# Kernel optimization log

Measured on AMD Instinct MI355X. Metric: run time of the kernel, lower is better.

## Reference

```python
import jax, jax.numpy as jnp
import numpy as np

IGNORE_INDEX = -100
LABEL_SMOOTH = 0.1
GAMMA = 2.0
MARGIN = 0.6
SENTENCE_SCALE = 0.1
K = 1000000.0
VOCAB = 32000
B, T = 4, 512


def setup_inputs() -> dict:
    key = jax.random.key(0)
    k1, k2, k3, k4 = jax.random.split(key, 4)
    inp = jax.random.normal(k1, (B, VOCAB, T), dtype=jnp.float32)
    weight = jax.random.uniform(k2, (VOCAB,), dtype=jnp.float32)
    target = jax.random.randint(k3, (B, T), 0, VOCAB, dtype=jnp.int64)
    seq_len = jax.random.randint(k4, (B,), 1, T, dtype=jnp.int64)
    return {"input": inp, "weight": weight, "target": target, "seq_len": seq_len}


def reference(input, weight, target, seq_len):
    V = weight.shape[0]
    b, t = target.shape
    # log-softmax / softmax over vocab dim (axis=1) -- single stable pass
    logp = jax.nn.log_softmax(input, axis=1)          # (B, V, T)
    prob = jnp.exp(logp)                              # == softmax(input, dim=1)
    tgt = target[:, None, :]                          # (B, 1, T)
    # probability of the gold token at each position
    occur_prob = jnp.take_along_axis(prob, tgt, axis=1)[:, 0, :]   # (B, T)
    # predicted token and correctness
    pred = jnp.argmax(input, axis=1)                  # (B, T)
    pred_true = pred == target
    # token occurrence counts (scatter-add) and correct-prediction counts
    flat_tgt = target.reshape(-1)
    all_count = jnp.zeros((V,), jnp.int32).at[flat_tgt].add(1)
    true_count = jnp.zeros((V,), jnp.int32).at[flat_tgt].add(pred_true.reshape(-1).astype(jnp.int32))
    all_count = all_count.at[IGNORE_INDEX].set(0)     # negative index, matches torch
    true_count = true_count.at[IGNORE_INDEX].set(0)
    # label-smoothed cross entropy
    nll = -jnp.take_along_axis(logp, tgt, axis=1)[:, 0, :]          # (B, T)
    false_mean = (-jnp.sum(logp, axis=1) - nll) / (V - 1)           # mean over non-target classes
    ignore_mask = (target != IGNORE_INDEX).astype(logp.dtype)
    loss = (nll * (1.0 - LABEL_SMOOTH) + false_mean * LABEL_SMOOTH) * ignore_mask
    # per-token class weight (max_scale_rate > 0 branch)
    loss = loss * weight[target]
    # focal factor
    loss = loss * (1.0 - occur_prob) ** GAMMA
    # sentence weight (sentence_scale < 1 branch)
    pad = jnp.arange(t)[None, :] >= seq_len[:, None]                # (B, T) padding mask
    sw = jax.nn.sigmoid(K * (MARGIN - occur_prob))
    sw = jnp.where(pad, 0.0, sw).max(axis=1)
    sw = jnp.clip(sw, SENTENCE_SCALE, 1.0)
    loss = loss * sw[:, None]
    return loss, true_count, all_count
```

## Files before the change

### kernel.cpp

```cpp
#include <hip/hip_runtime.h>
#include <math.h>

#define IGNORE_INDEX (-100)
constexpr int Bn   = 4;
constexpr int T    = 512;
constexpr int V    = 32000;
constexpr int COLS = Bn * T;
constexpr int NCH  = 256;
constexpr int CHUNK = V / NCH;
constexpr float LS     = 0.1f;
constexpr float MARGIN = 0.6f;
constexpr float SSCALE = 0.1f;
constexpr float KBIG   = 1000000.0f;

typedef float floatx2 __attribute__((ext_vector_type(2)));

__global__ __launch_bounds__(256) void kA(const float* __restrict__ in,
                                          float4* __restrict__ part,
                                          float* __restrict__ cnt_base) {
    int tg = blockIdx.x * 256 + threadIdx.x;
    if (tg < 2 * V) cnt_base[tg] = 0.f;

    int j  = tg >> 10;
    int g  = tg & 1023;
    int b  = g >> 8;
    int t  = (g & 255) << 1;

    const float* base = in + ((size_t)b * V + (size_t)j * CHUNK) * T + t;

    float m0 = -INFINITY, m1 = -INFINITY;
    float s0 = 0.f, s1 = 0.f;
    float x0 = 0.f, x1 = 0.f;
    int   i0 = 0, i1 = 0;

    int vbase = j * CHUNK;
    for (int i = 0; i < CHUNK - 5; i += 10) {
        floatx2 vv[10];
#pragma unroll
        for (int u = 0; u < 10; ++u)
            vv[u] = __builtin_nontemporal_load((const floatx2*)(base + (size_t)(i + u) * T));
#pragma unroll
        for (int u = 0; u < 10; ++u) {
            floatx2 v = vv[u];
            int vi = vbase + i + u;
            s0 += __expf(v.x); if (v.x > m0) { m0 = v.x; i0 = vi; } x0 += v.x;
            s1 += __expf(v.y); if (v.y > m1) { m1 = v.y; i1 = vi; } x1 += v.y;
        }
    }
    {
        floatx2 vv[5];
#pragma unroll
        for (int u = 0; u < 5; ++u)
            vv[u] = __builtin_nontemporal_load((const floatx2*)(base + (size_t)(120 + u) * T));
#pragma unroll
        for (int u = 0; u < 5; ++u) {
            floatx2 v = vv[u];
            int vi = vbase + 120 + u;
            s0 += __expf(v.x); if (v.x > m0) { m0 = v.x; i0 = vi; } x0 += v.x;
            s1 += __expf(v.y); if (v.y > m1) { m1 = v.y; i1 = vi; } x1 += v.y;
        }
    }

    int c0 = g * 2;
    part[(size_t)(c0 + 0) * NCH + j] = make_float4(m0, s0, x0, __int_as_float(i0));
    part[(size_t)(c0 + 1) * NCH + j] = make_float4(m1, s1, x1, __int_as_float(i1));
}

__device__ __forceinline__ float4 merge(float4 a, float4 b) {
    float m = fmaxf(a.x, b.x);
    int idx = (b.x > a.x) ? __float_as_int(b.w) : __float_as_int(a.w);
    return make_float4(m, a.y + b.y, a.z + b.z, __int_as_float(idx));
}

__global__ __launch_bounds__(64) void kB(const float4* __restrict__ part,
                                         const float* __restrict__ in,
                                         const float* __restrict__ wgt,
                                         const int*   __restrict__ tgt,
                                         float* __restrict__ loss_base,
                                         float* __restrict__ sig_arr,
                                         float* __restrict__ cnt_true,
                                         float* __restrict__ cnt_all) {
    int c   = blockIdx.x;
    int tid = threadIdx.x;

    int tg  = tgt[c];
    int b   = c >> 9;
    int t   = c & 511;
    int tgc = (tg < 0) ? 0 : tg;
    float xt = in[((size_t)b * V + (size_t)tgc) * T + t];
    float w  = wgt[tgc];

    const float4* p = part + (size_t)c * NCH + tid * 4;
    float4 r = merge(merge(p[0], p[1]), merge(p[2], p[3]));

#pragma unroll
    for (int off = 32; off > 0; off >>= 1) {
        float mx = __shfl_down(r.x, off, 64);
        float sy = __shfl_down(r.y, off, 64);
        float sz = __shfl_down(r.z, off, 64);
        float iw = __shfl_down(r.w, off, 64);
        float m  = fmaxf(r.x, mx);
        int  idx = (mx > r.x) ? __float_as_int(iw) : __float_as_int(r.w);
        r = make_float4(m, r.y + sy, r.z + sz, __int_as_float(idx));
    }

    if (tid == 0) {
        float s = r.y, sumx = r.z;
        int pred = __float_as_int(r.w);

        float Z = __logf(s);
        float xv = (tg == IGNORE_INDEX) ? 0.f : xt;
        float nll = Z - xv;
        float occur = __expf(xv - Z);
        float sum_logp = sumx - (float)V * Z;
        float false_mean = (-sum_logp - nll) / (float)(V - 1);

        float mask = (tg != IGNORE_INDEX) ? 1.f : 0.f;
        float ww = (tg == IGNORE_INDEX) ? 0.f : w;
        float om = 1.f - occur;
        float loss = (nll * (1.f - LS) + false_mean * LS) * mask * ww * om * om;
        loss_base[c] = loss;

        if (tg != IGNORE_INDEX) {
            atomicAdd(&cnt_all[tg], 1.0f);
            if (pred == tg) atomicAdd(&cnt_true[tg], 1.0f);
        }

        float z = KBIG * (MARGIN - occur);
        float sig = (z >= 0.f) ? 1.f / (1.f + __expf(-z))
                               : __expf(z) / (1.f + __expf(z));
        sig_arr[c] = sig;
    }
}

__global__ __launch_bounds__(512) void kC(const float* __restrict__ loss_base,
                                          const float* __restrict__ sig_arr,
                                          const int*   __restrict__ slen,
                                          float* __restrict__ out) {
    __shared__ float red[8];
    int b = blockIdx.x;
    int t = threadIdx.x;
    int c = (b << 9) + t;

    float v = (t < slen[b]) ? sig_arr[c] : 0.f;
#pragma unroll
    for (int off = 32; off > 0; off >>= 1)
        v = fmaxf(v, __shfl_down(v, off, 64));
    if ((t & 63) == 0) red[t >> 6] = v;
    __syncthreads();
    if (t == 0) {
        float m = red[0];
#pragma unroll
        for (int i = 1; i < 8; ++i) m = fmaxf(m, red[i]);
        red[0] = fminf(fmaxf(m, SSCALE), 1.0f);
    }
    __syncthreads();
    float sw = red[0];
    out[c] = loss_base[c] * sw;

    if (b == 0 && t == 0) {
        out[COLS + (V + IGNORE_INDEX)] = 0.f;
        out[COLS + V + (V + IGNORE_INDEX)] = 0.f;
    }
}

extern "C" void kernel_launch(void* const* d_in, const int* in_sizes, int n_in,
                              void* d_out, int out_size, void* d_ws, size_t ws_size,
                              hipStream_t stream) {
    const float* inp  = (const float*)d_in[0];
    const float* wgt  = (const float*)d_in[1];
    const int*   tgt  = (const int*)d_in[2];
    const int*   slen = (const int*)d_in[3];

    float* out = (float*)d_out;
    float* cnt_true = out + COLS;
    float* cnt_all  = out + COLS + V;

    float4* part = (float4*)d_ws;
    float* loss_base = (float*)((char*)d_ws + (size_t)COLS * NCH * sizeof(float4));
    float* sig_arr   = loss_base + COLS;

    kA<<<(COLS / 2) * NCH / 256, 256, 0, stream>>>(inp, part, cnt_true);
    kB<<<COLS, 64, 0, stream>>>(part, inp, wgt, tgt,
                                loss_base, sig_arr, cnt_true, cnt_all);
    kC<<<Bn, 512, 0, stream>>>(loss_base, sig_arr, slen, out);
}
```

Before: 343.4 us.

## Widen loads to float4 per thread, use 64-row chunks with double-buffered loads

Each kA thread now handles four adjacent columns with 16-byte nontemporal loads over 64-row vocab chunks, software-pipelined across two 8-deep register buffers. Vocab is split into 500 real chunks padded to 512, with neutral partials written for the padding. kB merges 8 partials per lane instead of 4. This aims to raise memory-load efficiency and overlap loads with exp/argmax math. In exchange it doubles the partials buffer, adds more partial traffic, and raises register pressure.

```diff
diff --git a/kernel.cpp b/kernel.cpp
--- a/kernel.cpp
+++ b/kernel.cpp
@@ -6,64 +6,86 @@
 constexpr int T    = 512;
 constexpr int V    = 32000;
 constexpr int COLS = Bn * T;
-constexpr int NCH  = 256;
-constexpr int CHUNK = V / NCH;
+constexpr int NCHR = 500;
+constexpr int NCHP = 512;
+constexpr int CH   = 64;
 constexpr float LS     = 0.1f;
 constexpr float MARGIN = 0.6f;
 constexpr float SSCALE = 0.1f;
 constexpr float KBIG   = 1000000.0f;
 
-typedef float floatx2 __attribute__((ext_vector_type(2)));
-
-__global__ __launch_bounds__(256) void kA(const float* __restrict__ in,
-                                          float4* __restrict__ part,
-                                          float* __restrict__ cnt_base) {
+typedef float floatx4 __attribute__((ext_vector_type(4)));
+
+__global__ __launch_bounds__(256, 4) void kA(const float* __restrict__ in,
+                                             floatx4* __restrict__ part,
+                                             float* __restrict__ cnt_base) {
     int tg = blockIdx.x * 256 + threadIdx.x;
     if (tg < 2 * V) cnt_base[tg] = 0.f;
 
-    int j  = tg >> 10;
-    int g  = tg & 1023;
-    int b  = g >> 8;
-    int t  = (g & 255) << 1;
-
-    const float* base = in + ((size_t)b * V + (size_t)j * CHUNK) * T + t;
-
-    float m0 = -INFINITY, m1 = -INFINITY;
-    float s0 = 0.f, s1 = 0.f;
-    float x0 = 0.f, x1 = 0.f;
-    int   i0 = 0, i1 = 0;
-
-    int vbase = j * CHUNK;
-    for (int i = 0; i < CHUNK - 5; i += 10) {
-        floatx2 vv[10];
-#pragma unroll
-        for (int u = 0; u < 10; ++u)
-            vv[u] = __builtin_nontemporal_load((const floatx2*)(base + (size_t)(i + u) * T));
-#pragma unroll
-        for (int u = 0; u < 10; ++u) {
-            floatx2 v = vv[u];
-            int vi = vbase + i + u;
-            s0 += __expf(v.x); if (v.x > m0) { m0 = v.x; i0 = vi; } x0 += v.x;
-            s1 += __expf(v.y); if (v.y > m1) { m1 = v.y; i1 = vi; } x1 += v.y;
-        }
-    }
-    {
-        floatx2 vv[5];
-#pragma unroll
-        for (int u = 0; u < 5; ++u)
-            vv[u] = __builtin_nontemporal_load((const floatx2*)(base + (size_t)(120 + u) * T));
-#pragma unroll
-        for (int u = 0; u < 5; ++u) {
-            floatx2 v = vv[u];
-            int vi = vbase + 120 + u;
-            s0 += __expf(v.x); if (v.x > m0) { m0 = v.x; i0 = vi; } x0 += v.x;
-            s1 += __expf(v.y); if (v.y > m1) { m1 = v.y; i1 = vi; } x1 += v.y;
-        }
-    }
-
-    int c0 = g * 2;
-    part[(size_t)(c0 + 0) * NCH + j] = make_float4(m0, s0, x0, __int_as_float(i0));
-    part[(size_t)(c0 + 1) * NCH + j] = make_float4(m1, s1, x1, __int_as_float(i1));
+    int j  = tg >> 9;
+    int g  = tg & 511;
+    int c0 = g << 2;
+
+    if (j >= NCHR) {
+        floatx4 neut = {-INFINITY, 0.f, 0.f, 0.f};
+#pragma unroll
+        for (int k = 0; k < 4; ++k)
+            part[(size_t)(c0 + k) * NCHP + j] = neut;
+        return;
+    }
+
+    int b = g >> 7;
+    int t = (g & 127) << 2;
+
+    const float* base = in + ((size_t)b * V + (size_t)j * CH) * T + t;
+
+    float m0=-INFINITY, m1=-INFINITY, m2=-INFINITY, m3=-INFINITY;
+    float s0=0.f, s1=0.f, s2=0.f, s3=0.f;
+    float x0=0.f, x1=0.f, x2=0.f, x3=0.f;
+    int   i0=0, i1=0, i2=0, i3=0;
+    int   vb = j * CH;
+
+    floatx4 bufA[8], bufB[8];
+
+#define LD(BUF, R0)                                                          \
+    _Pragma("unroll")                                                        \
+    for (int u = 0; u < 8; ++u)                                              \
+        BUF[u] = __builtin_nontemporal_load(                                 \
+            (const floatx4*)(base + (size_t)((R0) + u) * T));
+
+#define PR(BUF, R0)                                                          \
+    _Pragma("unroll")                                                        \
+    for (int u = 0; u < 8; ++u) {                                            \
+        floatx4 v = BUF[u];                                                  \
+        int vi = vb + (R0) + u;                                              \
+        s0 += __expf(v.x); if (v.x > m0) { m0 = v.x; i0 = vi; } x0 += v.x;   \
+        s1 += __expf(v.y); if (v.y > m1) { m1 = v.y; i1 = vi; } x1 += v.y;   \
+        s2 += __expf(v.z); if (v.z > m2) { m2 = v.z; i2 = vi; } x2 += v.z;   \
+        s3 += __expf(v.w); if (v.w > m3) { m3 = v.w; i3 = vi; } x3 += v.w;   \
+    }
+
+    LD(bufA, 0)
+    LD(bufB, 8)
+    PR(bufA, 0)   LD(bufA, 16)
+    PR(bufB, 8)   LD(bufB, 24)
+    PR(bufA, 16)  LD(bufA, 32)
+    PR(bufB, 24)  LD(bufB, 40)
+    PR(bufA, 32)  LD(bufA, 48)
+    PR(bufB, 40)  LD(bufB, 56)
+    PR(bufA, 48)
+    PR(bufB, 56)
+
+#undef LD
+#undef PR
+
+    floatx4 r0 = {m0, s0, x0, __int_as_float(i0)};
+    floatx4 r1 = {m1, s1, x1, __int_as_float(i1)};
+    floatx4 r2 = {m2, s2, x2, __int_as_float(i2)};
+    floatx4 r3 = {m3, s3, x3, __int_as_float(i3)};
+    part[(size_t)(c0 + 0) * NCHP + j] = r0;
+    part[(size_t)(c0 + 1) * NCHP + j] = r1;
+    part[(size_t)(c0 + 2) * NCHP + j] = r2;
+    part[(size_t)(c0 + 3) * NCHP + j] = r3;
 }
 
 __device__ __forceinline__ float4 merge(float4 a, float4 b) {
@@ -90,8 +112,10 @@
     float xt = in[((size_t)b * V + (size_t)tgc) * T + t];
     float w  = wgt[tgc];
 
-    const float4* p = part + (size_t)c * NCH + tid * 4;
-    float4 r = merge(merge(p[0], p[1]), merge(p[2], p[3]));
+    const float4* p = part + (size_t)c * NCHP + tid * 8;
+    float4 r = p[0];
+#pragma unroll
+    for (int k = 1; k < 8; ++k) r = merge(r, p[k]);
 
 #pragma unroll
     for (int off = 32; off > 0; off >>= 1) {
@@ -176,12 +200,12 @@
     float* cnt_true = out + COLS;
     float* cnt_all  = out + COLS + V;
 
-    float4* part = (float4*)d_ws;
-    float* loss_base = (float*)((char*)d_ws + (size_t)COLS * NCH * sizeof(float4));
+    floatx4* part = (floatx4*)d_ws;
+    float* loss_base = (float*)((char*)d_ws + (size_t)COLS * NCHP * sizeof(floatx4));
     float* sig_arr   = loss_base + COLS;
 
-    kA<<<(COLS / 2) * NCH / 256, 256, 0, stream>>>(inp, part, cnt_true);
-    kB<<<COLS, 64, 0, stream>>>(part, inp, wgt, tgt,
+    kA<<<(COLS / 4) * NCHP / 256, 256, 0, stream>>>(inp, part, cnt_true);
+    kB<<<COLS, 64, 0, stream>>>((const float4*)part, inp, wgt, tgt,
                                 loss_base, sig_arr, cnt_true, cnt_all);
     kC<<<Bn, 512, 0, stream>>>(loss_base, sig_arr, slen, out);
 }
```

New measurement: 355.6 us. 3.6% more time.

## Retile partial softmax pass into wave-wide 32-row chunks with double-buffered vector loads

Applied to the files above, without the earlier changes.

The first pass is remapped so each wavefront covers one batch and 32 vocab rows across all 512 positions. It uses 16-byte vector loads and a two-buffer software prefetch, and the launch bounds ask for 4 blocks per SIMD. Partials are stored chunk-major so the second pass can read them coalesced, with 8 columns per 256-thread block and a shared-memory reduction. The goal is to hide memory latency and widen loads. In exchange, the number of partial chunks grows from 256 to 1000, which quadruples the partial-buffer traffic and workspace size.

```diff
diff --git a/kernel.cpp b/kernel.cpp
--- a/kernel.cpp
+++ b/kernel.cpp
@@ -6,109 +6,134 @@
 constexpr int T    = 512;
 constexpr int V    = 32000;
 constexpr int COLS = Bn * T;
-constexpr int NCH  = 256;
-constexpr int CHUNK = V / NCH;
+constexpr int NJ   = 1000;
+constexpr int CH   = 32;
 constexpr float LS     = 0.1f;
 constexpr float MARGIN = 0.6f;
 constexpr float SSCALE = 0.1f;
 constexpr float KBIG   = 1000000.0f;
 
-typedef float floatx2 __attribute__((ext_vector_type(2)));
-
-__global__ __launch_bounds__(256) void kA(const float* __restrict__ in,
-                                          float4* __restrict__ part,
-                                          float* __restrict__ cnt_base) {
-    int tg = blockIdx.x * 256 + threadIdx.x;
-    if (tg < 2 * V) cnt_base[tg] = 0.f;
-
-    int j  = tg >> 10;
-    int g  = tg & 1023;
-    int b  = g >> 8;
-    int t  = (g & 255) << 1;
-
-    const float* base = in + ((size_t)b * V + (size_t)j * CHUNK) * T + t;
-
-    float m0 = -INFINITY, m1 = -INFINITY;
-    float s0 = 0.f, s1 = 0.f;
-    float x0 = 0.f, x1 = 0.f;
-    int   i0 = 0, i1 = 0;
-
-    int vbase = j * CHUNK;
-    for (int i = 0; i < CHUNK - 5; i += 10) {
-        floatx2 vv[10];
-#pragma unroll
-        for (int u = 0; u < 10; ++u)
-            vv[u] = __builtin_nontemporal_load((const floatx2*)(base + (size_t)(i + u) * T));
-#pragma unroll
-        for (int u = 0; u < 10; ++u) {
-            floatx2 v = vv[u];
-            int vi = vbase + i + u;
-            s0 += __expf(v.x); if (v.x > m0) { m0 = v.x; i0 = vi; } x0 += v.x;
-            s1 += __expf(v.y); if (v.y > m1) { m1 = v.y; i1 = vi; } x1 += v.y;
+typedef float floatx4 __attribute__((ext_vector_type(4)));
+
+__global__ __launch_bounds__(256, 4) void kA(const float* __restrict__ in,
+                                             float4* __restrict__ part,
+                                             float* __restrict__ cnt_base) {
+    int tid = blockIdx.x * 256 + threadIdx.x;
+    if (tid < 2 * V) cnt_base[tid] = 0.f;
+
+    int w = tid >> 6;
+    int l = tid & 63;
+    int b = w / 1000;
+    int j = w - b * 1000;
+
+    const float* base = in + ((size_t)b * V + (size_t)j * CH) * T + (l << 2);
+    int vb = j * CH;
+
+    float m[8], s[8], x[8]; int idx[8];
+#pragma unroll
+    for (int a = 0; a < 8; ++a) { m[a] = -INFINITY; s[a] = 0.f; x[a] = 0.f; idx[a] = 0; }
+
+    floatx4 bufA[8], bufB[8];
+
+#define LD(BUF, R0)                                                           \
+    _Pragma("unroll")                                                         \
+    for (int u = 0; u < 4; ++u) {                                             \
+        BUF[u*2+0] = *(const floatx4*)(base + (size_t)((R0) + u) * T);        \
+        BUF[u*2+1] = *(const floatx4*)(base + (size_t)((R0) + u) * T + 256);  \
+    }
+
+#define PR(BUF, R0)                                                           \
+    _Pragma("unroll")                                                         \
+    for (int u = 0; u < 4; ++u) {                                             \
+        int vi = vb + (R0) + u;                                               \
+        _Pragma("unroll")                                                     \
+        for (int h = 0; h < 2; ++h) {                                         \
+            floatx4 v = BUF[u*2+h];                                           \
+            _Pragma("unroll")                                                 \
+            for (int k = 0; k < 4; ++k) {                                     \
+                int a = h*4 + k;                                              \
+                float vv = v[k];                                              \
+                s[a] += __expf(vv);                                           \
+                if (vv > m[a]) { m[a] = vv; idx[a] = vi; }                    \
+                x[a] += vv;                                                   \
+            }                                                                 \
+        }                                                                     \
+    }
+
+    LD(bufA, 0)
+    LD(bufB, 4)
+    PR(bufA, 0)   LD(bufA, 8)
+    PR(bufB, 4)   LD(bufB, 12)
+    PR(bufA, 8)   LD(bufA, 16)
+    PR(bufB, 12)  LD(bufB, 20)
+    PR(bufA, 16)  LD(bufA, 24)
+    PR(bufB, 20)  LD(bufB, 28)
+    PR(bufA, 24)
+    PR(bufB, 28)
+
+#undef LD
+#undef PR
+
+#pragma unroll
+    for (int h = 0; h < 2; ++h)
+#pragma unroll
+        for (int k = 0; k < 4; ++k) {
+            int a = h*4 + k;
+            int c = b * T + h*256 + (l << 2) + k;
+            part[(size_t)j * COLS + c] =
+                make_float4(m[a], s[a], x[a], __int_as_float(idx[a]));
         }
-    }
-    {
-        floatx2 vv[5];
-#pragma unroll
-        for (int u = 0; u < 5; ++u)
-            vv[u] = __builtin_nontemporal_load((const floatx2*)(base + (size_t)(120 + u) * T));
-#pragma unroll
-        for (int u = 0; u < 5; ++u) {
-            floatx2 v = vv[u];
-            int vi = vbase + 120 + u;
-            s0 += __expf(v.x); if (v.x > m0) { m0 = v.x; i0 = vi; } x0 += v.x;
-            s1 += __expf(v.y); if (v.y > m1) { m1 = v.y; i1 = vi; } x1 += v.y;
-        }
-    }
-
-    int c0 = g * 2;
-    part[(size_t)(c0 + 0) * NCH + j] = make_float4(m0, s0, x0, __int_as_float(i0));
-    part[(size_t)(c0 + 1) * NCH + j] = make_float4(m1, s1, x1, __int_as_float(i1));
 }
 
 __device__ __forceinline__ float4 merge(float4 a, float4 b) {
     float m = fmaxf(a.x, b.x);
-    int idx = (b.x > a.x) ? __float_as_int(b.w) : __float_as_int(a.w);
-    return make_float4(m, a.y + b.y, a.z + b.z, __int_as_float(idx));
-}
-
-__global__ __launch_bounds__(64) void kB(const float4* __restrict__ part,
-                                         const float* __restrict__ in,
-                                         const float* __restrict__ wgt,
-                                         const int*   __restrict__ tgt,
-                                         float* __restrict__ loss_base,
-                                         float* __restrict__ sig_arr,
-                                         float* __restrict__ cnt_true,
-                                         float* __restrict__ cnt_all) {
-    int c   = blockIdx.x;
+    int idxv = (b.x > a.x) ? __float_as_int(b.w) : __float_as_int(a.w);
+    return make_float4(m, a.y + b.y, a.z + b.z, __int_as_float(idxv));
+}
+
+__global__ __launch_bounds__(256) void kB(const float4* __restrict__ part,
+                                          const float* __restrict__ in,
+                                          const float* __restrict__ wgt,
+                                          const int*   __restrict__ tgt,
+                                          float* __restrict__ loss_base,
+                                          float* __restrict__ sig_arr,
+                                          float* __restrict__ cnt_true,
+                                          float* __restrict__ cnt_all) {
+    __shared__ float4 sm[32][8];
+    int c0  = blockIdx.x * 8;
     int tid = threadIdx.x;
-
-    int tg  = tgt[c];
-    int b   = c >> 9;
-    int t   = c & 511;
-    int tgc = (tg < 0) ? 0 : tg;
-    float xt = in[((size_t)b * V + (size_t)tgc) * T + t];
-    float w  = wgt[tgc];
-
-    const float4* p = part + (size_t)c * NCH + tid * 4;
-    float4 r = merge(merge(p[0], p[1]), merge(p[2], p[3]));
-
-#pragma unroll
-    for (int off = 32; off > 0; off >>= 1) {
-        float mx = __shfl_down(r.x, off, 64);
-        float sy = __shfl_down(r.y, off, 64);
-        float sz = __shfl_down(r.z, off, 64);
-        float iw = __shfl_down(r.w, off, 64);
-        float m  = fmaxf(r.x, mx);
-        int  idx = (mx > r.x) ? __float_as_int(iw) : __float_as_int(r.w);
-        r = make_float4(m, r.y + sy, r.z + sz, __int_as_float(idx));
-    }
-
-    if (tid == 0) {
-        float s = r.y, sumx = r.z;
-        int pred = __float_as_int(r.w);
-
-        float Z = __logf(s);
+    int c_off = tid & 7, grp = tid >> 3;
+
+    int tg = 0; float xt = 0.f, wv = 0.f;
+    if (tid < 8) {
+        int c = c0 + tid;
+        tg = tgt[c];
+        int b = c >> 9, t = c & 511;
+        int tgc = (tg < 0) ? 0 : tg;
+        xt = in[((size_t)b * V + (size_t)tgc) * T + t];
+        wv = wgt[tgc];
+    }
+
+    float4 r = make_float4(-INFINITY, 0.f, 0.f, __int_as_float(0));
+    const float4* p = part + c0 + c_off;
+#pragma unroll 4
+    for (int jj = 0; jj < 32; ++jj) {
+        int j = grp * 32 + jj;
+        if (j < NJ) r = merge(r, p[(size_t)j * COLS]);
+    }
+    sm[grp][c_off] = r;
+    __syncthreads();
+
+    if (tid < 8) {
+        float4 r2 = sm[0][tid];
+#pragma unroll
+        for (int g = 1; g < 32; ++g) r2 = merge(r2, sm[g][tid]);
+
+        int c = c0 + tid;
+        float sum = r2.y, sumx = r2.z;
+        int pred = __float_as_int(r2.w);
+
+        float Z = __logf(sum);
         float xv = (tg == IGNORE_INDEX) ? 0.f : xt;
         float nll = Z - xv;
         float occur = __expf(xv - Z);
@@ -116,7 +141,7 @@
         float false_mean = (-sum_logp - nll) / (float)(V - 1);
 
         float mask = (tg != IGNORE_INDEX) ? 1.f : 0.f;
-        float ww = (tg == IGNORE_INDEX) ? 0.f : w;
+        float ww = (tg == IGNORE_INDEX) ? 0.f : wv;
         float om = 1.f - occur;
         float loss = (nll * (1.f - LS) + false_mean * LS) * mask * ww * om * om;
         loss_base[c] = loss;
@@ -177,11 +202,11 @@
     float* cnt_all  = out + COLS + V;
 
     float4* part = (float4*)d_ws;
-    float* loss_base = (float*)((char*)d_ws + (size_t)COLS * NCH * sizeof(float4));
+    float* loss_base = (float*)((char*)d_ws + (size_t)NJ * COLS * sizeof(float4));
     float* sig_arr   = loss_base + COLS;
 
-    kA<<<(COLS / 2) * NCH / 256, 256, 0, stream>>>(inp, part, cnt_true);
-    kB<<<COLS, 64, 0, stream>>>(part, inp, wgt, tgt,
-                                loss_base, sig_arr, cnt_true, cnt_all);
+    kA<<<1000, 256, 0, stream>>>(inp, part, cnt_true);
+    kB<<<COLS / 8, 256, 0, stream>>>(part, inp, wgt, tgt,
+                                     loss_base, sig_arr, cnt_true, cnt_all);
     kC<<<Bn, 512, 0, stream>>>(loss_base, sig_arr, slen, out);
 }
```

New measurement: 481.8 us. +40.3%, slower.
